# Kernel optimization log

Hardware: AMD Instinct MI355X
Metric: run time of the kernel (lower is better)

## Reference

```python
import jax, jax.numpy as jnp
import numpy as np

B, IN, H, M = 65536, 128, 256, 32


def setup_inputs() -> dict:
    key = jax.random.key(0)
    ks = jax.random.split(key, 8)
    s_i = 1.0 / np.sqrt(IN + H)
    s_m = 1.0 / np.sqrt(M)
    return {
        "input": jax.random.normal(ks[0], (B, IN), jnp.float32),
        "media": jax.random.normal(ks[1], (B, M), jnp.float32),
        "h_t": jax.random.normal(ks[2], (B, H), jnp.float32),
        "c_t": jax.random.normal(ks[3], (B, H), jnp.float32),
        "Wi": jax.random.normal(ks[4], (H, IN + H), jnp.float32) * s_i,
        "bi": jax.random.normal(ks[5], (H,), jnp.float32) * s_i,
        "Wm": jax.random.normal(ks[6], (H, M), jnp.float32) * s_m,
        "bm": jax.random.normal(ks[7], (H,), jnp.float32) * s_m,
    }


def reference(input, media, h_t, c_t, Wi, bi, Wm, bm):
    # original, so all gates share one pre-activation g.
    combined = jnp.concatenate([input, h_t], axis=1)
    g = combined @ Wi.T + bi                     # [B, H]
    gate = jax.nn.sigmoid(g)                     # i == f == o
    c = c_t * gate + jnp.tanh(g) * gate          # new cell state
    c_r = jnp.tanh(c)
    m = jax.nn.sigmoid(media @ Wm.T + bm)        # media gate [B, H]
    c_f = c - c_r + c_r * m
    h = jnp.tanh(c_f) * gate
    # classification=False -> output is h; returns (output, h, c)
    return (h, h, c)
```

## Files before the change

### kernel.cpp

```cpp
#include <hip/hip_runtime.h>

#define BB  65536
#define INW 128
#define HH  256
#define MM  32
#define KK  (INW + HH)
#define NKC 12

typedef __attribute__((ext_vector_type(8))) short bf16x8;
typedef __attribute__((ext_vector_type(4))) float f32x4;

__device__ __forceinline__ unsigned short f32_to_bf16(float f) {
    union { float f; unsigned u; } v; v.f = f;
    return (unsigned short)((v.u + 0x7fffu + ((v.u >> 16) & 1u)) >> 16);
}

__device__ __forceinline__ bf16x8 cvt8(f32x4 a, f32x4 b) {
    bf16x8 r;
    r[0] = (short)f32_to_bf16(a[0]); r[1] = (short)f32_to_bf16(a[1]);
    r[2] = (short)f32_to_bf16(a[2]); r[3] = (short)f32_to_bf16(a[3]);
    r[4] = (short)f32_to_bf16(b[0]); r[5] = (short)f32_to_bf16(b[1]);
    r[6] = (short)f32_to_bf16(b[2]); r[7] = (short)f32_to_bf16(b[3]);
    return r;
}

__device__ __forceinline__ float rcp_f(float x) { return __builtin_amdgcn_rcpf(x); }
__device__ __forceinline__ float sigmoid_f(float x) { return rcp_f(1.0f + __expf(-x)); }
__device__ __forceinline__ float tanh_f(float x) { return 1.0f - 2.0f * rcp_f(__expf(2.0f * x) + 1.0f); }

__global__ void pack_weights(const float* __restrict__ Wi, const float* __restrict__ Wm,
                             unsigned short* __restrict__ Wi_p, unsigned short* __restrict__ Wm_p) {
    int id = blockIdx.x * 256 + threadIdx.x;
    if (id < 2 * NKC * 8 * 512) {
        int blk = id >> 9;
        int e   = id & 511;
        int lane = e >> 3, j = e & 7;
        int lrow = lane & 15, quad = lane >> 4;
        int h  = blk / (NKC * 8);
        int b  = blk % (NKC * 8);
        int kc = b >> 3;
        int t  = b & 7;
        int n  = h * 128 + t * 16 + lrow;
        int k  = kc * 32 + quad * 8 + j;
        Wi_p[id] = f32_to_bf16(Wi[(size_t)n * KK + k]);
    }
    if (id < 2 * 8 * 512) {
        int blk = id >> 9;
        int e   = id & 511;
        int lane = e >> 3, j = e & 7;
        int lrow = lane & 15, quad = lane >> 4;
        int h = blk >> 3;
        int t = blk & 7;
        int n = h * 128 + t * 16 + lrow;
        Wm_p[id] = f32_to_bf16(Wm[(size_t)n * MM + quad * 8 + j]);
    }
}

__global__ __launch_bounds__(256) void rlstm_main(
    const float* __restrict__ input, const float* __restrict__ media,
    const float* __restrict__ h_t,   const float* __restrict__ c_t,
    const unsigned short* __restrict__ Wi_p, const float* __restrict__ bi,
    const unsigned short* __restrict__ Wm_p, const float* __restrict__ bm,
    float* __restrict__ out)
{
    const int tid  = threadIdx.x;
    const int wave = tid >> 6;
    const int lane = tid & 63;
    const int lrow = lane & 15;
    const int quad = lane >> 4;

    const int m0   = blockIdx.x * 32 + (wave >> 1) * 16;
    const int half = wave & 1;
    const int n0   = half * 128;

    const unsigned short* wip = Wi_p + (size_t)half * (NKC * 8 * 512);
    const unsigned short* wmp = Wm_p + (size_t)half * (8 * 512);

    const int arow = m0 + lrow;

    f32x4 md0 = *(const f32x4*)(media + (size_t)arow * MM + quad * 8);
    f32x4 md1 = *(const f32x4*)(media + (size_t)arow * MM + quad * 8 + 4);

    f32x4 accg[8];
#pragma unroll
    for (int t = 0; t < 8; ++t) accg[t] = (f32x4){0.f, 0.f, 0.f, 0.f};

#pragma unroll
    for (int kc = 0; kc < NKC; ++kc) {
        const float* src = (kc < 4)
            ? (input + (size_t)arow * INW + kc * 32 + quad * 8)
            : (h_t   + (size_t)arow * HH  + (kc - 4) * 32 + quad * 8);
        f32x4 a0 = ((const f32x4*)src)[0];
        f32x4 a1 = ((const f32x4*)src)[1];
        bf16x8 xf = cvt8(a0, a1);
        const unsigned short* wb = wip + (size_t)kc * (8 * 512) + lane * 8;
#pragma unroll
        for (int t = 0; t < 8; ++t) {
            bf16x8 wf = *(const bf16x8*)(wb + t * 512);
            accg[t] = __builtin_amdgcn_mfma_f32_16x16x32_bf16(wf, xf, accg[t], 0, 0, 0);
        }
    }

    bf16x8 mf = cvt8(md0, md1);
    const size_t outH = (size_t)BB * HH;
    const size_t rowbase = (size_t)arow * HH;
#pragma unroll
    for (int t = 0; t < 8; ++t) {
        bf16x8 wmf = *(const bf16x8*)(wmp + t * 512 + lane * 8);
        f32x4 am = __builtin_amdgcn_mfma_f32_16x16x32_bf16(
            wmf, mf, (f32x4){0.f, 0.f, 0.f, 0.f}, 0, 0, 0);

        const int nb = n0 + t * 16 + quad * 4;
        f32x4 bi4 = *(const f32x4*)(bi + nb);
        f32x4 bm4 = *(const f32x4*)(bm + nb);
        const size_t idx = rowbase + nb;
        f32x4 ct4 = *(const f32x4*)(c_t + idx);

        f32x4 h4, c4;
#pragma unroll
        for (int r = 0; r < 4; ++r) {
            float g    = accg[t][r] + bi4[r];
            float mp   = am[r] + bm4[r];
            float gate = sigmoid_f(g);
            float tg   = tanh_f(g);
            float c    = ct4[r] * gate + tg * gate;
            float cr   = tanh_f(c);
            float mg   = sigmoid_f(mp);
            float cf   = c - cr + cr * mg;
            float h    = tanh_f(cf) * gate;
            h4[r] = h; c4[r] = c;
        }
        *(f32x4*)(out + idx)            = h4;
        *(f32x4*)(out + idx + outH)     = h4;
        *(f32x4*)(out + idx + 2 * outH) = c4;
    }
}

extern "C" void kernel_launch(void* const* d_in, const int* in_sizes, int n_in,
                              void* d_out, int out_size, void* d_ws, size_t ws_size,
                              hipStream_t stream) {
    const float* input = (const float*)d_in[0];
    const float* media = (const float*)d_in[1];
    const float* h_t   = (const float*)d_in[2];
    const float* c_t   = (const float*)d_in[3];
    const float* Wi    = (const float*)d_in[4];
    const float* bi    = (const float*)d_in[5];
    const float* Wm    = (const float*)d_in[6];
    const float* bm    = (const float*)d_in[7];
    float* out = (float*)d_out;

    unsigned short* Wi_p = (unsigned short*)d_ws;
    unsigned short* Wm_p = Wi_p + 2 * NKC * 8 * 512;

    hipLaunchKernelGGL(pack_weights, dim3((2 * NKC * 8 * 512 + 255) / 256), dim3(256), 0, stream,
                       Wi, Wm, Wi_p, Wm_p);
    hipLaunchKernelGGL(rlstm_main, dim3(BB / 32), dim3(256), 0, stream,
                       input, media, h_t, c_t, Wi_p, bi, Wm_p, bm, out);
}
```

Measured before the change: 391.7 us.

## Process two 16-row M tiles per wave to reuse weight fragments; nontemporal I/O

Each wave now computes two 16-row batch tiles, so every loaded bf16 weight fragment feeds two MFMAs and weight traffic per output is halved. The grid shrinks to half as many blocks. The c_t loads and the three output stores now use nontemporal hints to avoid polluting cache with streaming data. This doubles accumulator registers per wave (64 floats), which may lower occupancy, and leaves fewer blocks to hide memory latency.

```diff
diff --git a/kernel.cpp b/kernel.cpp
--- a/kernel.cpp
+++ b/kernel.cpp
@@ -69,70 +69,90 @@
     const int lrow = lane & 15;
     const int quad = lane >> 4;
 
-    const int m0   = blockIdx.x * 32 + (wave >> 1) * 16;
     const int half = wave & 1;
+    const int m0   = blockIdx.x * 64 + (wave >> 1) * 32;
     const int n0   = half * 128;
 
     const unsigned short* wip = Wi_p + (size_t)half * (NKC * 8 * 512);
     const unsigned short* wmp = Wm_p + (size_t)half * (8 * 512);
 
-    const int arow = m0 + lrow;
+    const int arowA = m0 + lrow;
+    const int arowB = m0 + 16 + lrow;
 
-    f32x4 md0 = *(const f32x4*)(media + (size_t)arow * MM + quad * 8);
-    f32x4 md1 = *(const f32x4*)(media + (size_t)arow * MM + quad * 8 + 4);
-
-    f32x4 accg[8];
+    f32x4 accA[8], accB[8];
 #pragma unroll
-    for (int t = 0; t < 8; ++t) accg[t] = (f32x4){0.f, 0.f, 0.f, 0.f};
+    for (int t = 0; t < 8; ++t) {
+        accA[t] = (f32x4){0.f, 0.f, 0.f, 0.f};
+        accB[t] = (f32x4){0.f, 0.f, 0.f, 0.f};
+    }
 
 #pragma unroll
     for (int kc = 0; kc < NKC; ++kc) {
-        const float* src = (kc < 4)
-            ? (input + (size_t)arow * INW + kc * 32 + quad * 8)
-            : (h_t   + (size_t)arow * HH  + (kc - 4) * 32 + quad * 8);
-        f32x4 a0 = ((const f32x4*)src)[0];
-        f32x4 a1 = ((const f32x4*)src)[1];
-        bf16x8 xf = cvt8(a0, a1);
+        const float* srcA = (kc < 4)
+            ? (input + (size_t)arowA * INW + kc * 32 + quad * 8)
+            : (h_t   + (size_t)arowA * HH  + (kc - 4) * 32 + quad * 8);
+        const float* srcB = (kc < 4)
+            ? (input + (size_t)arowB * INW + kc * 32 + quad * 8)
+            : (h_t   + (size_t)arowB * HH  + (kc - 4) * 32 + quad * 8);
+        f32x4 a0 = ((const f32x4*)srcA)[0];
+        f32x4 a1 = ((const f32x4*)srcA)[1];
+        f32x4 b0 = ((const f32x4*)srcB)[0];
+        f32x4 b1 = ((const f32x4*)srcB)[1];
+        bf16x8 xfA = cvt8(a0, a1);
+        bf16x8 xfB = cvt8(b0, b1);
         const unsigned short* wb = wip + (size_t)kc * (8 * 512) + lane * 8;
 #pragma unroll
         for (int t = 0; t < 8; ++t) {
             bf16x8 wf = *(const bf16x8*)(wb + t * 512);
-            accg[t] = __builtin_amdgcn_mfma_f32_16x16x32_bf16(wf, xf, accg[t], 0, 0, 0);
+            accA[t] = __builtin_amdgcn_mfma_f32_16x16x32_bf16(wf, xfA, accA[t], 0, 0, 0);
+            accB[t] = __builtin_amdgcn_mfma_f32_16x16x32_bf16(wf, xfB, accB[t], 0, 0, 0);
         }
     }
 
-    bf16x8 mf = cvt8(md0, md1);
+    bf16x8 mfA = cvt8(*(const f32x4*)(media + (size_t)arowA * MM + quad * 8),
+                      *(const f32x4*)(media + (size_t)arowA * MM + quad * 8 + 4));
+    bf16x8 mfB = cvt8(*(const f32x4*)(media + (size_t)arowB * MM + quad * 8),
+                      *(const f32x4*)(media + (size_t)arowB * MM + quad * 8 + 4));
     const size_t outH = (size_t)BB * HH;
-    const size_t rowbase = (size_t)arow * HH;
+    const size_t rowbaseA = (size_t)arowA * HH;
+    const size_t rowbaseB = (size_t)arowB * HH;
+
 #pragma unroll
     for (int t = 0; t < 8; ++t) {
         bf16x8 wmf = *(const bf16x8*)(wmp + t * 512 + lane * 8);
-        f32x4 am = __builtin_amdgcn_mfma_f32_16x16x32_bf16(
-            wmf, mf, (f32x4){0.f, 0.f, 0.f, 0.f}, 0, 0, 0);
+        f32x4 amA = __builtin_amdgcn_mfma_f32_16x16x32_bf16(
+            wmf, mfA, (f32x4){0.f, 0.f, 0.f, 0.f}, 0, 0, 0);
+        f32x4 amB = __builtin_amdgcn_mfma_f32_16x16x32_bf16(
+            wmf, mfB, (f32x4){0.f, 0.f, 0.f, 0.f}, 0, 0, 0);
 
         const int nb = n0 + t * 16 + quad * 4;
         f32x4 bi4 = *(const f32x4*)(bi + nb);
         f32x4 bm4 = *(const f32x4*)(bm + nb);
-        const size_t idx = rowbase + nb;
-        f32x4 ct4 = *(const f32x4*)(c_t + idx);
 
-        f32x4 h4, c4;
 #pragma unroll
-        for (int r = 0; r < 4; ++r) {
-            float g    = accg[t][r] + bi4[r];
-            float mp   = am[r] + bm4[r];
-            float gate = sigmoid_f(g);
-            float tg   = tanh_f(g);
-            float c    = ct4[r] * gate + tg * gate;
-            float cr   = tanh_f(c);
-            float mg   = sigmoid_f(mp);
-            float cf   = c - cr + cr * mg;
-            float h    = tanh_f(cf) * gate;
-            h4[r] = h; c4[r] = c;
+        for (int mt = 0; mt < 2; ++mt) {
+            const size_t idx = (mt ? rowbaseB : rowbaseA) + nb;
+            const f32x4* accp = mt ? accB : accA;
+            const f32x4  am   = mt ? amB : amA;
+            f32x4 ct4 = __builtin_nontemporal_load((const f32x4*)(c_t + idx));
+            f32x4 h4, c4;
+#pragma unroll
+            for (int r = 0; r < 4; ++r) {
+                float g    = accp[t][r] + bi4[r];
+                float mp   = am[r] + bm4[r];
+                float gate = sigmoid_f(g);
+                float tg   = tanh_f(g);
+                float c    = ct4[r] * gate + tg * gate;
+                float cr   = tanh_f(c);
+                float mg   = sigmoid_f(mp);
+                float cf   = c - cr + cr * mg;
+                float h    = tanh_f(cf) * gate;
+                h4[r] = h; c4[r] = c;
+            }
+            __builtin_nontemporal_store(h4, (f32x4*)(out + idx));
+            __builtin_nontemporal_store(h4, (f32x4*)(out + idx + outH));
+            __builtin_nontemporal_store(c4, (f32x4*)(out + idx + 2 * outH));
         }
-        *(f32x4*)(out + idx)            = h4;
-        *(f32x4*)(out + idx + outH)     = h4;
-        *(f32x4*)(out + idx + 2 * outH) = c4;
     }
 }
 
@@ -154,6 +174,6 @@
 
     hipLaunchKernelGGL(pack_weights, dim3((2 * NKC * 8 * 512 + 255) / 256), dim3(256), 0, stream,
                        Wi, Wm, Wi_p, Wm_p);
-    hipLaunchKernelGGL(rlstm_main, dim3(BB / 32), dim3(256), 0, stream,
+    hipLaunchKernelGGL(rlstm_main, dim3(BB / 64), dim3(256), 0, stream,
                        input, media, h_t, c_t, Wi_p, bi, Wm_p, bm, out);
 }
```

New measurement: 430.4 us. 1.1x slower.
